# Kernel optimization log

Hardware: AMD Instinct MI355X
Metric: run time of the kernel (lower is better)

Reference implementation:

```python
import jax, jax.numpy as jnp
import numpy as np
from jax import lax

K = 3            # kernel size
KP = K * K       # kernel_size_prod
CENTER = KP // 2 # center tap index
PIXEL_SIZE = 1.0
DILATION = 1


def _unfold(x):
    # torch F.unfold equivalent: [N, C*KP, oh, ow] with channel-major, spatial-minor tap order
    return lax.conv_general_dilated_patches(
        x, filter_shape=(K, K), window_strides=(1, 1),
        padding=((1, 1), (1, 1)), rhs_dilation=(DILATION, DILATION))


def setup_inputs() -> dict:
    key = jax.random.key(0)
    ks = jax.random.split(key, 6)
    N, C, O, H, W = 8, 128, 128, 64, 64
    x = jax.random.normal(ks[0], (N, C, H, W), jnp.float32)
    depth = jax.random.uniform(ks[1], (N, 1, H, W), jnp.float32)  # >0 almost surely
    fx = jax.random.uniform(ks[2], (N,), jnp.float32) + 0.5       # per-image focal scale
    s = 1.0 / np.sqrt(C * KP)
    w0 = jax.random.normal(ks[3], (O, C, K, K), jnp.float32) * s
    w1 = jax.random.normal(ks[4], (O, C, K, K), jnp.float32) * s
    w2 = jax.random.normal(ks[5], (O, C, K, K), jnp.float32) * s
    return {"x": x, "depth": depth, "fx": fx, "w0": w0, "w1": w1, "w2": w2}


def reference(x, depth, fx, w0, w1, w2):
    N, C, H, W = x.shape
    O = w0.shape[0]
    patches = _unfold(x)                      # [N, C*9, oh, ow]
    oh, ow = patches.shape[2], patches.shape[3]
    L = oh * ow
    x_col = patches.reshape(N, C, KP, L)       # [N, C, 9, L]
    d_col = _unfold(depth).reshape(N, KP, L)   # [N, 9, L]

    valid = (d_col != 0.0).astype(jnp.float32)
    valid = valid * valid[:, CENTER:CENTER + 1, :]
    d_col = d_col * valid
    center = d_col[:, CENTER:CENTER + 1, :]    # [N, 1, L]
    grid = PIXEL_SIZE * DILATION * center / fx[:, None, None]
    half = grid * 0.5

    m0 = (jnp.abs(d_col - (center + grid)) <= half).astype(jnp.float32)
    m1 = (jnp.abs(d_col - center) <= half).astype(jnp.float32)
    m1 = jnp.clip(m1 + 1.0 - valid, 0.0, 1.0)
    m2 = (jnp.abs(d_col - (center - grid)) <= half).astype(jnp.float32)

    def branch(w, m):
        # (O, C*9) @ (N, C*9, L) as an einsum over (C, tap)
        return jnp.einsum('ock,nckl->nol', w.reshape(O, C, KP), x_col * m[:, None])

    out = branch(w0, m0) + branch(w1, m1) + branch(w2, m2)
    return out.reshape(N, O, oh, ow)
```

## Files before the change

kernel.cpp:

```cpp
#include <hip/hip_runtime.h>
#include <hip/hip_bf16.h>
#include <cstdint>
#include <cstddef>

#define Nn 8
#define Cc 128
#define Oo 128
#define Hh 64
#define Ww 64
#define LL (Hh * Ww)
#define KP 9

typedef __attribute__((ext_vector_type(8))) short short8;
typedef __attribute__((ext_vector_type(4))) float floatx4;
typedef __attribute__((ext_vector_type(4))) int intx4;

#define SGB(m, s, i) __builtin_amdgcn_sched_group_barrier(m, s, i)

__device__ __forceinline__ unsigned short f2bf(float f) {
  unsigned int u = __float_as_uint(f);
  u += 0x7fffu + ((u >> 16) & 1u);
  return (unsigned short)(u >> 16);
}

__global__ __launch_bounds__(256) void prep_all(const float* __restrict__ x,
                                                const float* __restrict__ w0,
                                                const float* __restrict__ w1,
                                                const float* __restrict__ w2,
                                                const float* __restrict__ depth,
                                                const float* __restrict__ fx,
                                                unsigned short* __restrict__ xt,
                                                unsigned short* __restrict__ wt2,
                                                unsigned int* __restrict__ codesg) {
  __shared__ float tile[Cc][Ww + 1];
  __shared__ unsigned short wl[Cc * KP];
  const int bid = blockIdx.x;
  const int t = threadIdx.x;
  if (bid < Nn * Hh) {
    const int n = bid >> 6;
    const int h = bid & 63;
    const float* src = x + (size_t)n * Cc * LL + (size_t)h * Ww;
#pragma unroll
    for (int it = 0; it < 8; ++it) {
      const int idx = t + it * 256;
      const int c = idx >> 4;
      const int w4 = (idx & 15) << 2;
      const float4 v = *reinterpret_cast<const float4*>(src + (size_t)c * LL + w4);
      tile[c][w4 + 0] = v.x; tile[c][w4 + 1] = v.y;
      tile[c][w4 + 2] = v.z; tile[c][w4 + 3] = v.w;
    }
    __syncthreads();
    unsigned short* dst = xt + (size_t)((n * Hh + h) * Ww) * Cc;
#pragma unroll
    for (int it = 0; it < 4; ++it) {
      const int idx = t + it * 256;
      const int w = idx >> 4;
      const int ch = (idx & 15) << 3;
      short8 v;
#pragma unroll
      for (int q = 0; q < 8; ++q)
        ((unsigned short*)&v)[q] = f2bf(tile[ch + q][w]);
      *reinterpret_cast<short8*>(dst + (size_t)w * Cc + ch) = v;
    }
  } else if (bid < Nn * Hh + 3 * Oo) {
    const int bo = bid - Nn * Hh;
    const int b = bo >> 7;
    const int o = bo & 127;
    const float* w = (b == 0) ? w0 : (b == 1) ? w1 : w2;
    const float* src = w + (size_t)o * Cc * KP;
#pragma unroll
    for (int it = 0; it < 5; ++it) {
      const int idx = t + it * 256;
      if (idx < Cc * KP) wl[idx] = f2bf(src[idx]);
    }
    __syncthreads();
    const int obase = ((o >> 6) & 1) * 2048 + ((o >> 5) & 1) * 1024 +
                      ((o >> 4) & 1) * 512 + (o & 15) * 32;
#pragma unroll
    for (int it = 0; it < 5; ++it) {
      const int idx = t + it * 256;
      if (idx < Cc * KP) {
        const int kk = idx >> 7;
        const int c = idx & 127;
        const int c0 = c >> 5;
        const int cc = c & 31;
        wt2[(size_t)(b * 36 + kk * 4 + c0) * 4096 + obase + cc] = wl[c * KP + kk];
      }
    }
  } else {
    const int p = (bid - (Nn * Hh + 3 * Oo)) * 256 + t;
    const int n = p >> 12;
    const int rem = p & 4095;
    const int h = rem >> 6;
    const int w = rem & 63;
    const float center = depth[p];
    const float grid = center / fx[n];
    const float half = 0.5f * grid;
    unsigned int packed = 0u;
#pragma unroll
    for (int kk = 0; kk < KP; ++kk) {
      const int hh = h + kk / 3 - 1;
      const int ww = w + kk % 3 - 1;
      float d = 0.0f;
      if (hh >= 0 && hh < Hh && ww >= 0 && ww < Ww) d = depth[(n << 12) + hh * Ww + ww];
      const float valid = (d != 0.0f && center != 0.0f) ? 1.0f : 0.0f;
      const float dm = d * valid;
      unsigned int cb = 0u;
      if (fabsf(dm - (center + grid)) <= half) cb |= 1u;
      float m1v = (fabsf(dm - center) <= half) ? 1.0f : 0.0f;
      m1v = m1v + 1.0f - valid;
      if (m1v > 1.0f) m1v = 1.0f;
      if (m1v > 0.5f) cb |= 2u;
      if (fabsf(dm - (center - grid)) <= half) cb |= 4u;
      packed |= cb << (3 * kk);
    }
    codesg[p] = packed;
  }
}

#define LDXC 132
#define HALO_COLS 66
#define HALO_ROWS 4
#define NSTEP 18
#define BSTRIDE 147456

__global__ __launch_bounds__(256, 2) void conv_main(
    const unsigned short* __restrict__ xt,
    const unsigned short* __restrict__ wt2,
    const unsigned int* __restrict__ codesg,
    float* __restrict__ out) {
  __shared__ __align__(16) unsigned short Xs[HALO_ROWS * HALO_COLS * LDXC];

  const int g = blockIdx.x;
  const int n = g >> 6;
  const int rem = g & 63;
  const int pb = rem >> 1;
  const int ob1 = rem & 1;
  const int h0 = pb * 2;

  const int tid = threadIdx.x;
  const int lane = tid & 63;
  const int wave = tid >> 6;
  const int ln15 = lane & 15;
  const int quad = lane >> 4;
  const int wc = wave & 1;
  const int ks = wave >> 1;

  const unsigned short* wfragk =
      wt2 + (size_t)(ob1 * 2048 + wc * 1024 + ln15 * 32 + quad * 8) + (size_t)ks * 8192;
  const int xbase = quad * 8 + ks * 64;

  short8 Bb[3][6];
  short8 Aa[2][8];

#define LOADB(SLOT, S)                                                            \
  {                                                                               \
    const unsigned short* bp = wfragk + (size_t)((((S) >> 1) * 4) + ((S) & 1)) * 4096; \
    Bb[SLOT][0] = *reinterpret_cast<const short8*>(bp);                           \
    Bb[SLOT][1] = *reinterpret_cast<const short8*>(bp + 512);                     \
    Bb[SLOT][2] = *reinterpret_cast<const short8*>(bp + BSTRIDE);                 \
    Bb[SLOT][3] = *reinterpret_cast<const short8*>(bp + BSTRIDE + 512);           \
    Bb[SLOT][4] = *reinterpret_cast<const short8*>(bp + 2 * BSTRIDE);             \
    Bb[SLOT][5] = *reinterpret_cast<const short8*>(bp + 2 * BSTRIDE + 512);       \
  }

#define LOADA(SLOT, S)                                                            \
  {                                                                               \
    const int kkp = (S) >> 1;                                                     \
    const int dyp = kkp / 3, dxp = kkp % 3;                                       \
    _Pragma("unroll")                                                             \
    for (int i = 0; i < 8; ++i) {                                                 \
      const int pix = ((i >> 2) + dyp) * HALO_COLS + (i & 3) * 16 + ln15 + dxp;   \
      Aa[SLOT][i] = *reinterpret_cast<const short8*>(&Xs[pix * LDXC + ((S) & 1) * 32 + xbase]); \
    }                                                                             \
  }

  LOADB(0, 0)
  LOADB(1, 1)

  unsigned int cd[8];
  {
    const unsigned int* cp = codesg + (n << 12) + h0 * 64 + ln15;
#pragma unroll
    for (int i = 0; i < 8; ++i) cd[i] = cp[i * 16];
  }

#pragma unroll
  for (int it = 0; it < 17; ++it) {
    const int idx = tid + it * 256;
    if (idx < HALO_ROWS * HALO_COLS * 16) {
      const int ch = (idx & 15) << 3;
      const int pixidx = idx >> 4;
      const int lc = pixidx % HALO_COLS;
      const int hrel = pixidx / HALO_COLS;
      const int hh = h0 - 1 + hrel;
      const int ww = lc - 1;
      short8 v = {0, 0, 0, 0, 0, 0, 0, 0};
      if (hh >= 0 && hh < Hh && ww >= 0 && ww < Ww)
        v = *reinterpret_cast<const short8*>(
            xt + (size_t)((n * Hh + hh) * Ww + ww) * Cc + ch);
      *reinterpret_cast<short8*>(&Xs[pixidx * LDXC + ch]) = v;
    }
  }

  __syncthreads();

  const floatx4 zf4 = {0.f, 0.f, 0.f, 0.f};
  floatx4 acc[8][2];
#pragma unroll
  for (int i = 0; i < 8; ++i)
#pragma unroll
    for (int j = 0; j < 2; ++j) acc[i][j] = zf4;

  LOADA(0, 0)

#pragma unroll
  for (int s = 0; s < NSTEP; ++s) {
    if (s + 2 < NSTEP) LOADB((s + 2) % 3, s + 2)
    if (s + 1 < NSTEP) LOADA((s + 1) & 1, s + 1)
    const int kk = s >> 1;
    const int shift = 3 * kk;
    const short8* B = Bb[s % 3];
    const short8* A = Aa[s & 1];
#pragma unroll
    for (int b = 0; b < 3; ++b) {
#pragma unroll
      for (int i = 0; i < 8; ++i) {
        const int msk = __builtin_amdgcn_sbfe((int)cd[i], shift + b, 1);
        intx4 a4 = *reinterpret_cast<const intx4*>(&A[i]);
        intx4 m4 = {msk, msk, msk, msk};
        a4 &= m4;
        const short8 af = *reinterpret_cast<const short8*>(&a4);
        acc[i][0] = __builtin_amdgcn_mfma_f32_16x16x32_bf16(af, B[b * 2 + 0], acc[i][0], 0, 0, 0);
        acc[i][1] = __builtin_amdgcn_mfma_f32_16x16x32_bf16(af, B[b * 2 + 1], acc[i][1], 0, 0, 0);
      }
    }
    SGB(0x020, 1, 0); SGB(0x008, 4, 0); SGB(0x100, 1, 0); SGB(0x008, 4, 0);
    SGB(0x020, 1, 0); SGB(0x008, 4, 0); SGB(0x100, 1, 0); SGB(0x008, 4, 0);
    SGB(0x020, 1, 0); SGB(0x008, 4, 0); SGB(0x100, 1, 0); SGB(0x008, 4, 0);
    SGB(0x020, 1, 0); SGB(0x008, 4, 0); SGB(0x100, 1, 0); SGB(0x008, 4, 0);
    SGB(0x020, 1, 0); SGB(0x008, 4, 0); SGB(0x100, 1, 0); SGB(0x008, 4, 0);
    SGB(0x020, 1, 0); SGB(0x008, 4, 0); SGB(0x100, 3, 0); SGB(0x008, 4, 0);
  }

  __syncthreads();
  float* scratch = reinterpret_cast<float*>(Xs);
  if (ks == 1) {
#pragma unroll
    for (int i = 0; i < 8; ++i)
#pragma unroll
      for (int j = 0; j < 2; ++j) {
        const int tile = (wc * 16 + i * 2 + j) * 64 + lane;
        *reinterpret_cast<floatx4*>(&scratch[tile * 4]) = acc[i][j];
      }
  }
  __syncthreads();
  if (ks == 0) {
#pragma unroll
    for (int i = 0; i < 8; ++i) {
      const int m = i * 16 + quad * 4;
      const int h = h0 + (m >> 6);
      const int w = m & 63;
#pragma unroll
      for (int j = 0; j < 2; ++j) {
        const int tile = (wc * 16 + i * 2 + j) * 64 + lane;
        const floatx4 other = *reinterpret_cast<const floatx4*>(&scratch[tile * 4]);
        const floatx4 sum = acc[i][j] + other;
        const int o = ob1 * 64 + wc * 32 + j * 16 + ln15;
        float* dst = out + (size_t)(n * Oo + o) * LL + h * Ww + w;
        *reinterpret_cast<floatx4*>(dst) = sum;
      }
    }
  }
}

extern "C" void kernel_launch(void* const* d_in, const int* in_sizes, int n_in,
                              void* d_out, int out_size, void* d_ws, size_t ws_size,
                              hipStream_t stream) {
  const float* x     = (const float*)d_in[0];
  const float* depth = (const float*)d_in[1];
  const float* fx    = (const float*)d_in[2];
  const float* w0    = (const float*)d_in[3];
  const float* w1    = (const float*)d_in[4];
  const float* w2    = (const float*)d_in[5];
  float* out = (float*)d_out;

  unsigned short* xt = (unsigned short*)d_ws;
  unsigned short* wt2 = xt + (size_t)Nn * Hh * Ww * Cc;
  unsigned int* codesg = (unsigned int*)(wt2 + (size_t)3 * KP * Oo * Cc);

  prep_all<<<Nn * Hh + 3 * Oo + 128, 256, 0, stream>>>(x, w0, w1, w2, depth, fx, xt, wt2, codesg);
  conv_main<<<512, 256, 0, stream>>>(xt, wt2, codesg, out);
}
```

Before: 109.3 us.

## Switch conv GEMM from 16x16x32 to 32x32x16 bf16 MFMA tiles

Replaces the 16x16x32 MFMA tiling with 32x32x16 MFMA instructions. The weight layout written by the prep kernel, the A/B fragment loads from LDS and global memory, the mask extraction and the epilogue are all reindexed to match the 32-row/32-column fragment shape. Larger MFMA tiles mean fewer instructions and fewer mask/AND operations per FLOP, and more operand reuse per load. The cost is a different register footprint and LDS access pattern, plus re-tuned sched_group_barrier groupings that may not interleave as well.

```diff
diff --git a/kernel.cpp b/kernel.cpp
--- a/kernel.cpp
+++ b/kernel.cpp
@@ -13,6 +13,7 @@
 
 typedef __attribute__((ext_vector_type(8))) short short8;
 typedef __attribute__((ext_vector_type(4))) float floatx4;
+typedef __attribute__((ext_vector_type(16))) float f32x16;
 typedef __attribute__((ext_vector_type(4))) int intx4;
 
 #define SGB(m, s, i) __builtin_amdgcn_sched_group_barrier(m, s, i)
@@ -74,17 +75,14 @@
       if (idx < Cc * KP) wl[idx] = f2bf(src[idx]);
     }
     __syncthreads();
-    const int obase = ((o >> 6) & 1) * 2048 + ((o >> 5) & 1) * 1024 +
-                      ((o >> 4) & 1) * 512 + (o & 15) * 32;
 #pragma unroll
     for (int it = 0; it < 5; ++it) {
       const int idx = t + it * 256;
       if (idx < Cc * KP) {
         const int kk = idx >> 7;
         const int c = idx & 127;
-        const int c0 = c >> 5;
-        const int cc = c & 31;
-        wt2[(size_t)(b * 36 + kk * 4 + c0) * 4096 + obase + cc] = wl[c * KP + kk];
+        wt2[(size_t)(((b * 9 + kk) * 16 + (c >> 3)) * 128 + o) * 8 + (c & 7)] =
+            wl[c * KP + kk];
       }
     }
   } else {
@@ -122,7 +120,6 @@
 #define HALO_COLS 66
 #define HALO_ROWS 4
 #define NSTEP 18
-#define BSTRIDE 147456
 
 __global__ __launch_bounds__(256, 2) void conv_main(
     const unsigned short* __restrict__ xt,
@@ -141,48 +138,51 @@
   const int tid = threadIdx.x;
   const int lane = tid & 63;
   const int wave = tid >> 6;
-  const int ln15 = lane & 15;
-  const int quad = lane >> 4;
+  const int l31 = lane & 31;
+  const int lg = lane >> 5;
   const int wc = wave & 1;
   const int ks = wave >> 1;
 
-  const unsigned short* wfragk =
-      wt2 + (size_t)(ob1 * 2048 + wc * 1024 + ln15 * 32 + quad * 8) + (size_t)ks * 8192;
-  const int xbase = quad * 8 + ks * 64;
+  const unsigned short* wf =
+      wt2 + ((size_t)(ks * 8 + lg) * 128 + ob1 * 64 + wc * 32 + l31) * 8;
 
   short8 Bb[3][6];
   short8 Aa[2][8];
 
-#define LOADB(SLOT, S)                                                            \
-  {                                                                               \
-    const unsigned short* bp = wfragk + (size_t)((((S) >> 1) * 4) + ((S) & 1)) * 4096; \
-    Bb[SLOT][0] = *reinterpret_cast<const short8*>(bp);                           \
-    Bb[SLOT][1] = *reinterpret_cast<const short8*>(bp + 512);                     \
-    Bb[SLOT][2] = *reinterpret_cast<const short8*>(bp + BSTRIDE);                 \
-    Bb[SLOT][3] = *reinterpret_cast<const short8*>(bp + BSTRIDE + 512);           \
-    Bb[SLOT][4] = *reinterpret_cast<const short8*>(bp + 2 * BSTRIDE);             \
-    Bb[SLOT][5] = *reinterpret_cast<const short8*>(bp + 2 * BSTRIDE + 512);       \
-  }
-
-#define LOADA(SLOT, S)                                                            \
-  {                                                                               \
-    const int kkp = (S) >> 1;                                                     \
-    const int dyp = kkp / 3, dxp = kkp % 3;                                       \
-    _Pragma("unroll")                                                             \
-    for (int i = 0; i < 8; ++i) {                                                 \
-      const int pix = ((i >> 2) + dyp) * HALO_COLS + (i & 3) * 16 + ln15 + dxp;   \
-      Aa[SLOT][i] = *reinterpret_cast<const short8*>(&Xs[pix * LDXC + ((S) & 1) * 32 + xbase]); \
-    }                                                                             \
+#define LOADB(SLOT, S)                                                               \
+  {                                                                                  \
+    const int kkq = (S) >> 1, hfq = (S) & 1;                                         \
+    _Pragma("unroll")                                                                \
+    for (int kc = 0; kc < 2; ++kc)                                                   \
+      _Pragma("unroll")                                                              \
+      for (int b = 0; b < 3; ++b)                                                    \
+        Bb[SLOT][kc * 3 + b] = *reinterpret_cast<const short8*>(                     \
+            wf + (size_t)(((b * 9 + kkq) * 16 + hfq * 4 + kc * 2)) * 1024);          \
+  }
+
+#define LOADA(SLOT, S)                                                               \
+  {                                                                                  \
+    const int kkp = (S) >> 1, hfp = (S) & 1;                                         \
+    const int dyp = kkp / 3, dxp = kkp % 3;                                          \
+    _Pragma("unroll")                                                                \
+    for (int mt = 0; mt < 4; ++mt)                                                   \
+      _Pragma("unroll")                                                              \
+      for (int kc = 0; kc < 2; ++kc) {                                               \
+        const int pix = ((mt >> 1) + dyp) * HALO_COLS + (mt & 1) * 32 + l31 + dxp;   \
+        const int coff = ks * 64 + hfp * 32 + kc * 16 + lg * 8;                      \
+        Aa[SLOT][mt * 2 + kc] =                                                      \
+            *reinterpret_cast<const short8*>(&Xs[pix * LDXC + coff]);                \
+      }                                                                              \
   }
 
   LOADB(0, 0)
   LOADB(1, 1)
 
-  unsigned int cd[8];
+  unsigned int cd2[4];
   {
-    const unsigned int* cp = codesg + (n << 12) + h0 * 64 + ln15;
-#pragma unroll
-    for (int i = 0; i < 8; ++i) cd[i] = cp[i * 16];
+    const unsigned int* cp = codesg + (n << 12) + h0 * 64;
+#pragma unroll
+    for (int mt = 0; mt < 4; ++mt) cd2[mt] = cp[mt * 32 + l31];
   }
 
 #pragma unroll
@@ -205,12 +205,11 @@
 
   __syncthreads();
 
-  const floatx4 zf4 = {0.f, 0.f, 0.f, 0.f};
-  floatx4 acc[8][2];
-#pragma unroll
-  for (int i = 0; i < 8; ++i)
-#pragma unroll
-    for (int j = 0; j < 2; ++j) acc[i][j] = zf4;
+  f32x16 acc2[4];
+#pragma unroll
+  for (int mt = 0; mt < 4; ++mt)
+    acc2[mt] = (f32x16){0.f, 0.f, 0.f, 0.f, 0.f, 0.f, 0.f, 0.f,
+                        0.f, 0.f, 0.f, 0.f, 0.f, 0.f, 0.f, 0.f};
 
   LOADA(0, 0)
 
@@ -224,49 +223,59 @@
     const short8* A = Aa[s & 1];
 #pragma unroll
     for (int b = 0; b < 3; ++b) {
-#pragma unroll
-      for (int i = 0; i < 8; ++i) {
-        const int msk = __builtin_amdgcn_sbfe((int)cd[i], shift + b, 1);
-        intx4 a4 = *reinterpret_cast<const intx4*>(&A[i]);
-        intx4 m4 = {msk, msk, msk, msk};
-        a4 &= m4;
-        const short8 af = *reinterpret_cast<const short8*>(&a4);
-        acc[i][0] = __builtin_amdgcn_mfma_f32_16x16x32_bf16(af, B[b * 2 + 0], acc[i][0], 0, 0, 0);
-        acc[i][1] = __builtin_amdgcn_mfma_f32_16x16x32_bf16(af, B[b * 2 + 1], acc[i][1], 0, 0, 0);
+      int msk[4];
+#pragma unroll
+      for (int mt = 0; mt < 4; ++mt)
+        msk[mt] = __builtin_amdgcn_sbfe((int)cd2[mt], shift + b, 1);
+#pragma unroll
+      for (int kc = 0; kc < 2; ++kc) {
+#pragma unroll
+        for (int mt = 0; mt < 4; ++mt) {
+          intx4 a4 = *reinterpret_cast<const intx4*>(&A[mt * 2 + kc]);
+          intx4 m4 = {msk[mt], msk[mt], msk[mt], msk[mt]};
+          a4 &= m4;
+          const short8 af = *reinterpret_cast<const short8*>(&a4);
+          acc2[mt] = __builtin_amdgcn_mfma_f32_32x32x16_bf16(af, B[kc * 3 + b],
+                                                             acc2[mt], 0, 0, 0);
+        }
       }
     }
-    SGB(0x020, 1, 0); SGB(0x008, 4, 0); SGB(0x100, 1, 0); SGB(0x008, 4, 0);
-    SGB(0x020, 1, 0); SGB(0x008, 4, 0); SGB(0x100, 1, 0); SGB(0x008, 4, 0);
-    SGB(0x020, 1, 0); SGB(0x008, 4, 0); SGB(0x100, 1, 0); SGB(0x008, 4, 0);
-    SGB(0x020, 1, 0); SGB(0x008, 4, 0); SGB(0x100, 1, 0); SGB(0x008, 4, 0);
-    SGB(0x020, 1, 0); SGB(0x008, 4, 0); SGB(0x100, 1, 0); SGB(0x008, 4, 0);
-    SGB(0x020, 1, 0); SGB(0x008, 4, 0); SGB(0x100, 3, 0); SGB(0x008, 4, 0);
+    SGB(0x020, 1, 0); SGB(0x008, 2, 0); SGB(0x100, 1, 0); SGB(0x008, 2, 0);
+    SGB(0x020, 1, 0); SGB(0x008, 2, 0); SGB(0x100, 1, 0); SGB(0x008, 2, 0);
+    SGB(0x020, 1, 0); SGB(0x008, 2, 0); SGB(0x100, 1, 0); SGB(0x008, 2, 0);
+    SGB(0x020, 1, 0); SGB(0x008, 2, 0); SGB(0x100, 1, 0); SGB(0x008, 2, 0);
+    SGB(0x020, 1, 0); SGB(0x008, 2, 0); SGB(0x100, 1, 0); SGB(0x008, 2, 0);
+    SGB(0x020, 1, 0); SGB(0x008, 2, 0); SGB(0x100, 3, 0); SGB(0x008, 2, 0);
   }
 
   __syncthreads();
   float* scratch = reinterpret_cast<float*>(Xs);
   if (ks == 1) {
 #pragma unroll
-    for (int i = 0; i < 8; ++i)
-#pragma unroll
-      for (int j = 0; j < 2; ++j) {
-        const int tile = (wc * 16 + i * 2 + j) * 64 + lane;
-        *reinterpret_cast<floatx4*>(&scratch[tile * 4]) = acc[i][j];
+    for (int mt = 0; mt < 4; ++mt)
+#pragma unroll
+      for (int q4 = 0; q4 < 4; ++q4) {
+        const floatx4 v = {acc2[mt][q4 * 4 + 0], acc2[mt][q4 * 4 + 1],
+                           acc2[mt][q4 * 4 + 2], acc2[mt][q4 * 4 + 3]};
+        *reinterpret_cast<floatx4*>(
+            &scratch[(((wc * 4 + mt) * 4 + q4) * 64 + lane) * 4]) = v;
       }
   }
   __syncthreads();
   if (ks == 0) {
-#pragma unroll
-    for (int i = 0; i < 8; ++i) {
-      const int m = i * 16 + quad * 4;
-      const int h = h0 + (m >> 6);
-      const int w = m & 63;
-#pragma unroll
-      for (int j = 0; j < 2; ++j) {
-        const int tile = (wc * 16 + i * 2 + j) * 64 + lane;
-        const floatx4 other = *reinterpret_cast<const floatx4*>(&scratch[tile * 4]);
-        const floatx4 sum = acc[i][j] + other;
-        const int o = ob1 * 64 + wc * 32 + j * 16 + ln15;
+    const int o = ob1 * 64 + wc * 32 + l31;
+#pragma unroll
+    for (int mt = 0; mt < 4; ++mt) {
+      const int h = h0 + (mt >> 1);
+      const int wbase = (mt & 1) * 32;
+#pragma unroll
+      for (int q4 = 0; q4 < 4; ++q4) {
+        const floatx4 other = *reinterpret_cast<const floatx4*>(
+            &scratch[(((wc * 4 + mt) * 4 + q4) * 64 + lane) * 4]);
+        const floatx4 mine = {acc2[mt][q4 * 4 + 0], acc2[mt][q4 * 4 + 1],
+                              acc2[mt][q4 * 4 + 2], acc2[mt][q4 * 4 + 3]};
+        const floatx4 sum = mine + other;
+        const int w = wbase + q4 * 8 + lg * 4;
         float* dst = out + (size_t)(n * Oo + o) * LL + h * Ww + w;
         *reinterpret_cast<floatx4*>(dst) = sum;
       }
```

New measurement: 110.4 us. Within noise of the previous version (+1.0%).
